# Optimization experiments

Measured on AMD Instinct MI355X. Metric: run time of the kernel, lower is better.

Reference implementation:

```python
import jax, jax.numpy as jnp
import numpy as np

TEMPERATURE = 0.1
NEG_FILL = -9e15


def setup_inputs() -> dict:
    key = jax.random.key(0)
    k1, k2, k3, k4 = jax.random.split(key, 4)
    N, D = 2048, 256
    loc1 = jax.random.normal(k1, (N, D), dtype=jnp.float32)
    loc2 = jax.random.normal(k3, (N, D), dtype=jnp.float32)
    # variances must be positive; sample in [0.5, 1.5)
    scale1 = jax.random.uniform(k2, (N, D), dtype=jnp.float32, minval=0.5, maxval=1.5)
    scale2 = jax.random.uniform(k4, (N, D), dtype=jnp.float32, minval=0.5, maxval=1.5)
    return {"loc1": loc1, "scale1": scale1, "loc2": loc2, "scale2": scale2}


def _kl_loss(loc1, scale1, loc2, scale2):
    N, D = loc1.shape
    mu = jnp.concatenate([loc1, loc2], axis=0)    # [2N, D]
    var = jnp.concatenate([scale1, scale2], axis=0)  # [2N, D] (treated as variance)
    inv_var = 1.0 / var
    s_logvar = jnp.sum(jnp.log(var), axis=-1)      # [2N]
    # kld[i,j] = 0.5 * sum_d( logvar_j - logvar_i - 1 + ((mu_i-mu_j)^2 + var_i)/var_j )
    # expand (mu_i-mu_j)^2 = mu_i^2 - 2 mu_i mu_j + mu_j^2 -> three GEMM/reduction terms
    a = (mu * mu + var) @ inv_var.T                # [2N,2N]: sum_d (mu_i^2+var_i)/var_j
    b = mu @ (mu * inv_var).T                      # [2N,2N]: sum_d mu_i mu_j / var_j
    c = jnp.sum(mu * mu * inv_var, axis=-1)        # [2N]:    sum_d mu_j^2 / var_j
    kld = 0.5 * (s_logvar[None, :] - s_logvar[:, None]
                 - jnp.float32(D) + a - 2.0 * b + c[None, :])
    M = 2 * N
    idx = jnp.arange(M)
    kld = kld.at[idx, idx].set(NEG_FILL)           # fill_diagonal_(-9e15)
    sim = kld / TEMPERATURE
    pos = sim[idx, (idx - N) % M]                  # eye rolled by N along dim 0
    loss = jax.nn.logsumexp(sim, axis=-1) - pos
    return jnp.mean(loss)


def reference(loc1, scale1, loc2, scale2):
    return _kl_loss(loc1, scale1, loc2, scale2)
```

## Files before the change

kernel.cpp:

```cpp
#include <hip/hip_runtime.h>
#include <hip/hip_bf16.h>
#include <math.h>

#define N_HALF 2048
#define M_TOT  4096
#define D_DIM  256
#define K2     512
#define NBLK   16
#define NKT    8
#define TILE_BYTES 32768

typedef __attribute__((ext_vector_type(8))) short bf16x8;
typedef __attribute__((ext_vector_type(4))) float f32x4;

static __device__ __forceinline__ unsigned short f2bf(float x) {
    union { __hip_bfloat16 h; unsigned short u; } cv;
    cv.h = __float2bfloat16(x);
    return cv.u;
}

static __device__ __forceinline__ void gll16(const void* g, void* l) {
    __builtin_amdgcn_global_load_lds(
        (const __attribute__((address_space(1))) unsigned int*)g,
        (__attribute__((address_space(3))) unsigned int*)l, 16, 0, 0);
}

#define FENCE asm volatile("" ::: "memory")
#define BAR() do { FENCE; __builtin_amdgcn_s_barrier(); FENCE; } while (0)
#define VM(n) asm volatile("s_waitcnt vmcnt(" #n ")" ::: "memory")

__global__ __launch_bounds__(256) void prep_kernel(
        const float* __restrict__ loc1, const float* __restrict__ scale1,
        const float* __restrict__ loc2, const float* __restrict__ scale2,
        unsigned short* __restrict__ Ab, unsigned short* __restrict__ Bb,
        float* __restrict__ slv, float* __restrict__ cvec,
        float* __restrict__ out) {
    const int t = threadIdx.x, w = t >> 6, lane = t & 63;
    if (blockIdx.x == 0 && t == 0) out[0] = 0.0f;
    const int i = blockIdx.x * 4 + w;
    const float* mup  = (i < N_HALF) ? loc1 + (size_t)i * D_DIM   : loc2 + (size_t)(i - N_HALF) * D_DIM;
    const float* vap  = (i < N_HALF) ? scale1 + (size_t)i * D_DIM : scale2 + (size_t)(i - N_HALF) * D_DIM;
    const float4 mu = *(const float4*)(mup + lane * 4);
    const float4 va = *(const float4*)(vap + lane * 4);
    const float4 iv = {1.0f / va.x, 1.0f / va.y, 1.0f / va.z, 1.0f / va.w};

    float lacc = __logf(va.x * va.y * va.z * va.w);
    float cacc = mu.x * mu.x * iv.x + mu.y * mu.y * iv.y
               + mu.z * mu.z * iv.z + mu.w * mu.w * iv.w;
    #pragma unroll
    for (int off = 1; off < 64; off <<= 1) {
        lacc += __shfl_xor(lacc, off, 64);
        cacc += __shfl_xor(cacc, off, 64);
    }
    if (lane == 0) { slv[i] = lacc; cvec[i] = cacc; }

    const int by = i >> 8, r = i & 255;
    const int rsw = (r >> 1) & 3;
    char* const abase = (char*)Ab + (size_t)by * (NKT * TILE_BYTES) + r * 64;
    char* const bbase = (char*)Bb + (size_t)by * (NKT * TILE_BYTES) + r * 64;
    #define ST4(base, k, v0, v1, v2, v3)                                             \
        {   const int kk = (k);                                                      \
            const int kt = kk >> 6, ks = (kk >> 5) & 1;                              \
            const int sl = ((kk >> 3) & 3) ^ rsw, hf = (kk >> 2) & 1;                \
            ushort4 pk = {f2bf(v0), f2bf(v1), f2bf(v2), f2bf(v3)};                   \
            *(ushort4*)((base) + (size_t)kt * TILE_BYTES + ks * 16384                \
                        + sl * 16 + hf * 8) = pk; }
    ST4(abase, lane * 4,          mu.x * mu.x + va.x, mu.y * mu.y + va.y,
                                  mu.z * mu.z + va.z, mu.w * mu.w + va.w)
    ST4(abase, 256 + lane * 4,    -2.0f * mu.x, -2.0f * mu.y, -2.0f * mu.z, -2.0f * mu.w)
    ST4(bbase, lane * 4,          iv.x, iv.y, iv.z, iv.w)
    ST4(bbase, 256 + lane * 4,    mu.x * iv.x, mu.y * iv.y, mu.z * iv.z, mu.w * iv.w)
    #undef ST4
}

__global__ __launch_bounds__(512, 2) void gemm_lse_kernel(
        const unsigned short* __restrict__ Ab, const unsigned short* __restrict__ Bb,
        const float* __restrict__ slv, const float* __restrict__ cvec,
        float* __restrict__ pm, float* __restrict__ ps,
        float* __restrict__ pos) {
    extern __shared__ __align__(16) char smem[];
    const int t = threadIdx.x;
    const int lane = t & 63, wid = t >> 6;
    const int bx = blockIdx.x, by = blockIdx.y;
    const int wrow = wid >> 2, wcol = wid & 3;
    const int fr = lane & 15, g = lane >> 4;
    const int t16 = t * 16;

    int a_off[8][2], b_off[4][2];
    #pragma unroll
    for (int fm = 0; fm < 8; ++fm) {
        const int row = wrow * 128 + fm * 16 + fr;
        #pragma unroll
        for (int ks = 0; ks < 2; ++ks)
            a_off[fm][ks] = ks * 16384 + row * 64 + ((g ^ ((row >> 1) & 3)) << 4);
    }
    #pragma unroll
    for (int fn = 0; fn < 4; ++fn) {
        const int row = wcol * 64 + fn * 16 + fr;
        #pragma unroll
        for (int ks = 0; ks < 2; ++ks)
            b_off[fn][ks] = 32768 + ks * 16384 + row * 64 + ((g ^ ((row >> 1) & 3)) << 4);
    }

    f32x4 acc[8][4];
    #pragma unroll
    for (int i = 0; i < 8; ++i)
        #pragma unroll
        for (int j = 0; j < 4; ++j) acc[i][j] = (f32x4){0.f, 0.f, 0.f, 0.f};

    const char* gA = (const char*)Ab + (size_t)by * (NKT * TILE_BYTES);
    const char* gB = (const char*)Bb + (size_t)bx * (NKT * TILE_BYTES);

    #define S2(kt, ks, isB)                                                          \
        {   const char* _s = ((isB) ? gB : gA) + (size_t)(kt) * TILE_BYTES           \
                             + (ks) * 16384;                                         \
            char* _d = smem + ((kt) & 1) * 65536 + ((isB) ? 32768 : 0)               \
                       + (ks) * 16384;                                               \
            gll16(_s + t16, _d + t16);                                               \
            gll16(_s + 8192 + t16, _d + 8192 + t16); }

    S2(0, 0, 0) S2(0, 0, 1) S2(0, 1, 0) S2(0, 1, 1) S2(1, 0, 0) S2(1, 0, 1)
    VM(8);
    BAR();

    bf16x8 bfr[4], af[8];
    for (int kt = 0; kt < NKT; ++kt) {
        const char* bufc = smem + (kt & 1) * 65536;

        #define MFMA16(FMH)                                                          \
            __builtin_amdgcn_s_setprio(1);                                           \
            _Pragma("unroll")                                                        \
            for (int q = 0; q < 4; ++q) {                                            \
                acc[(FMH)*4+q][0] = __builtin_amdgcn_mfma_f32_16x16x32_bf16(af[(FMH)*4+q], bfr[0], acc[(FMH)*4+q][0], 0, 0, 0); \
                acc[(FMH)*4+q][1] = __builtin_amdgcn_mfma_f32_16x16x32_bf16(af[(FMH)*4+q], bfr[1], acc[(FMH)*4+q][1], 0, 0, 0); \
                acc[(FMH)*4+q][2] = __builtin_amdgcn_mfma_f32_16x16x32_bf16(af[(FMH)*4+q], bfr[2], acc[(FMH)*4+q][2], 0, 0, 0); \
                acc[(FMH)*4+q][3] = __builtin_amdgcn_mfma_f32_16x16x32_bf16(af[(FMH)*4+q], bfr[3], acc[(FMH)*4+q][3], 0, 0, 0); \
            }                                                                        \
            __builtin_amdgcn_s_setprio(0);

        if (kt + 1 < NKT) S2(kt + 1, 1, 0)
        #pragma unroll
        for (int q = 0; q < 4; ++q) bfr[q]    = *(const bf16x8*)(bufc + b_off[q][0]);
        #pragma unroll
        for (int q = 0; q < 8; ++q) af[q]     = *(const bf16x8*)(bufc + a_off[q][0]);
        if (kt + 1 < NKT) S2(kt + 1, 1, 1)
        MFMA16(0)
        MFMA16(1)
        if (kt + 1 < NKT) { VM(8); } else { VM(0); }
        BAR();

        if (kt + 2 < NKT) S2(kt + 2, 0, 0)
        #pragma unroll
        for (int q = 0; q < 4; ++q) bfr[q]    = *(const bf16x8*)(bufc + b_off[q][1]);
        #pragma unroll
        for (int q = 0; q < 8; ++q) af[q]     = *(const bf16x8*)(bufc + a_off[q][1]);
        if (kt + 2 < NKT) S2(kt + 2, 0, 1)
        MFMA16(0)
        MFMA16(1)
        if (kt + 2 < NKT)      { VM(8); }
        else if (kt + 1 < NKT) { VM(4); }
        BAR();
        #undef MFMA16
    }
    #undef S2

    float colv[4]; int gcol[4];
    #pragma unroll
    for (int fn = 0; fn < 4; ++fn) {
        const int c = bx * 256 + wcol * 64 + fn * 16 + fr;
        gcol[fn] = c;
        colv[fn] = 5.0f * (slv[c] + cvec[c]) - 1280.0f;
    }
    float* redm = (float*)smem;
    float* reds = (float*)(smem + 4096);

    #pragma unroll
    for (int fm = 0; fm < 8; ++fm) {
        #pragma unroll
        for (int q = 0; q < 4; ++q) {
            const int rloc = wrow * 128 + fm * 16 + g * 4 + q;
            const int grow = by * 256 + rloc;
            const int jpart = grow ^ N_HALF;
            float v[4];
            #pragma unroll
            for (int fn = 0; fn < 4; ++fn) {
                const float x = 5.0f * acc[fm][fn][q] + colv[fn];
                if (gcol[fn] == jpart) pos[grow] = x;
                v[fn] = (grow == gcol[fn]) ? -3.0e38f : x;
            }
            float m = fmaxf(fmaxf(v[0], v[1]), fmaxf(v[2], v[3]));
            #pragma unroll
            for (int off = 1; off < 16; off <<= 1) m = fmaxf(m, __shfl_xor(m, off, 64));
            float s = __expf(v[0] - m) + __expf(v[1] - m) + __expf(v[2] - m) + __expf(v[3] - m);
            #pragma unroll
            for (int off = 1; off < 16; off <<= 1) s += __shfl_xor(s, off, 64);
            if (fr == 0) { redm[rloc * 4 + wcol] = m; reds[rloc * 4 + wcol] = s; }
        }
    }
    __syncthreads();
    if (t < 256) {
        float m = redm[t * 4], s = reds[t * 4];
        #pragma unroll
        for (int k = 1; k < 4; ++k) {
            const float mk = redm[t * 4 + k], sk = reds[t * 4 + k];
            const float nm = fmaxf(m, mk);
            s = s * __expf(m - nm) + sk * __expf(mk - nm);
            m = nm;
        }
        pm[(size_t)(by * 256 + t) * NBLK + bx] = m;
        ps[(size_t)(by * 256 + t) * NBLK + bx] = s;
    }
}

__global__ __launch_bounds__(256) void finalize_kernel(
        const float* __restrict__ pm, const float* __restrict__ ps,
        const float* __restrict__ pos, float* __restrict__ out) {
    __shared__ float sm[256];
    const int t = threadIdx.x;
    const int i = blockIdx.x * 256 + t;
    float mk[NBLK];
    float m = -3.0e38f;
    #pragma unroll
    for (int k = 0; k < NBLK; ++k) {
        mk[k] = pm[(size_t)i * NBLK + k];
        m = fmaxf(m, mk[k]);
    }
    float s = 0.0f;
    #pragma unroll
    for (int k = 0; k < NBLK; ++k)
        s += ps[(size_t)i * NBLK + k] * __expf(mk[k] - m);
    sm[t] = m + logf(s) - pos[i];
    __syncthreads();
    for (int off = 128; off > 0; off >>= 1) {
        if (t < off) sm[t] += sm[t + off];
        __syncthreads();
    }
    if (t == 0) atomicAdd(out, sm[0] * (1.0f / (float)M_TOT));
}

extern "C" void kernel_launch(void* const* d_in, const int* in_sizes, int n_in,
                              void* d_out, int out_size, void* d_ws, size_t ws_size,
                              hipStream_t stream) {
    const float* loc1   = (const float*)d_in[0];
    const float* scale1 = (const float*)d_in[1];
    const float* loc2   = (const float*)d_in[2];
    const float* scale2 = (const float*)d_in[3];
    float* out = (float*)d_out;

    char* ws = (char*)d_ws;
    unsigned short* Ab = (unsigned short*)ws;
    unsigned short* Bb = (unsigned short*)(ws + (size_t)4 * 1024 * 1024);
    float* slv  = (float*)(ws + (size_t)8 * 1024 * 1024);
    float* cvec = slv + M_TOT;
    float* pm   = cvec + M_TOT;
    float* ps   = pm + (size_t)M_TOT * NBLK;
    float* pos  = ps + (size_t)M_TOT * NBLK;

    hipLaunchKernelGGL(prep_kernel, dim3(M_TOT / 4), dim3(256), 0, stream,
                       loc1, scale1, loc2, scale2, Ab, Bb, slv, cvec, out);
    hipLaunchKernelGGL(gemm_lse_kernel, dim3(NBLK, NBLK), dim3(512), 131072, stream,
                       Ab, Bb, slv, cvec, pm, ps, pos);
    hipLaunchKernelGGL(finalize_kernel, dim3(NBLK), dim3(256), 0, stream,
                       pm, ps, pos, out);
}
```

Baseline: 42.30 us.

## Halve GEMM row tile, use 3-stage K pipeline and swizzled block order

The GEMM block tile changes from 256x256 to 128x256 with a K step of 32, doubling the grid to 512 blocks. Loads now go through a triple-buffered LDS ring of 24KB stages, and launch bounds rise to 4 blocks per CU. The prep kernel's packed bf16 layout is rewritten to match, and blocks are remapped so neighbouring blocks share B column tiles. The aim is to fill the 256 CUs better and hide load latency, at the cost of lower per-block reuse and more barriers per unit of work.

```diff
diff --git a/kernel.cpp b/kernel.cpp
--- a/kernel.cpp
+++ b/kernel.cpp
@@ -7,8 +7,11 @@
 #define D_DIM  256
 #define K2     512
 #define NBLK   16
-#define NKT    8
-#define TILE_BYTES 32768
+#define NKT    16
+#define A_TB   8192
+#define B_TB   16384
+#define BUF_B  24576
+#define NROWB  32
 
 typedef __attribute__((ext_vector_type(8))) short bf16x8;
 typedef __attribute__((ext_vector_type(4))) float f32x4;
@@ -54,26 +57,24 @@
     }
     if (lane == 0) { slv[i] = lacc; cvec[i] = cacc; }
 
-    const int by = i >> 8, r = i & 255;
-    const int rsw = (r >> 1) & 3;
-    char* const abase = (char*)Ab + (size_t)by * (NKT * TILE_BYTES) + r * 64;
-    char* const bbase = (char*)Bb + (size_t)by * (NKT * TILE_BYTES) + r * 64;
-    #define ST4(base, k, v0, v1, v2, v3)                                             \
+    const int rsw = (i >> 1) & 3;
+    char* const abase = (char*)Ab + (size_t)(i >> 7) * (NKT * A_TB) + (i & 127) * 64;
+    char* const bbase = (char*)Bb + (size_t)(i >> 8) * (NKT * B_TB) + (i & 255) * 64;
+    #define ST4(base, TB, k, v0, v1, v2, v3)                                         \
         {   const int kk = (k);                                                      \
-            const int kt = kk >> 6, ks = (kk >> 5) & 1;                              \
+            const int kt = kk >> 5;                                                  \
             const int sl = ((kk >> 3) & 3) ^ rsw, hf = (kk >> 2) & 1;                \
             ushort4 pk = {f2bf(v0), f2bf(v1), f2bf(v2), f2bf(v3)};                   \
-            *(ushort4*)((base) + (size_t)kt * TILE_BYTES + ks * 16384                \
-                        + sl * 16 + hf * 8) = pk; }
-    ST4(abase, lane * 4,          mu.x * mu.x + va.x, mu.y * mu.y + va.y,
-                                  mu.z * mu.z + va.z, mu.w * mu.w + va.w)
-    ST4(abase, 256 + lane * 4,    -2.0f * mu.x, -2.0f * mu.y, -2.0f * mu.z, -2.0f * mu.w)
-    ST4(bbase, lane * 4,          iv.x, iv.y, iv.z, iv.w)
-    ST4(bbase, 256 + lane * 4,    mu.x * iv.x, mu.y * iv.y, mu.z * iv.z, mu.w * iv.w)
+            *(ushort4*)((base) + (size_t)kt * (TB) + sl * 16 + hf * 8) = pk; }
+    ST4(abase, A_TB, lane * 4,       mu.x * mu.x + va.x, mu.y * mu.y + va.y,
+                                     mu.z * mu.z + va.z, mu.w * mu.w + va.w)
+    ST4(abase, A_TB, 256 + lane * 4, -2.0f * mu.x, -2.0f * mu.y, -2.0f * mu.z, -2.0f * mu.w)
+    ST4(bbase, B_TB, lane * 4,       iv.x, iv.y, iv.z, iv.w)
+    ST4(bbase, B_TB, 256 + lane * 4, mu.x * iv.x, mu.y * iv.y, mu.z * iv.z, mu.w * iv.w)
     #undef ST4
 }
 
-__global__ __launch_bounds__(512, 2) void gemm_lse_kernel(
+__global__ __launch_bounds__(512, 4) void gemm_lse_kernel(
         const unsigned short* __restrict__ Ab, const unsigned short* __restrict__ Bb,
         const float* __restrict__ slv, const float* __restrict__ cvec,
         float* __restrict__ pm, float* __restrict__ ps,
@@ -81,88 +82,72 @@
     extern __shared__ __align__(16) char smem[];
     const int t = threadIdx.x;
     const int lane = t & 63, wid = t >> 6;
-    const int bx = blockIdx.x, by = blockIdx.y;
+    const int bid = blockIdx.x;
+    const int swz = ((bid & 7) << 6) | (bid >> 3);
+    const int bx = swz >> 5, by2 = swz & 31;
     const int wrow = wid >> 2, wcol = wid & 3;
     const int fr = lane & 15, g = lane >> 4;
     const int t16 = t * 16;
 
-    int a_off[8][2], b_off[4][2];
-    #pragma unroll
-    for (int fm = 0; fm < 8; ++fm) {
-        const int row = wrow * 128 + fm * 16 + fr;
-        #pragma unroll
-        for (int ks = 0; ks < 2; ++ks)
-            a_off[fm][ks] = ks * 16384 + row * 64 + ((g ^ ((row >> 1) & 3)) << 4);
+    int a_off[4], b_off[4];
+    #pragma unroll
+    for (int fm = 0; fm < 4; ++fm) {
+        const int row = wrow * 64 + fm * 16 + fr;
+        a_off[fm] = row * 64 + ((g ^ ((row >> 1) & 3)) << 4);
     }
     #pragma unroll
     for (int fn = 0; fn < 4; ++fn) {
         const int row = wcol * 64 + fn * 16 + fr;
-        #pragma unroll
-        for (int ks = 0; ks < 2; ++ks)
-            b_off[fn][ks] = 32768 + ks * 16384 + row * 64 + ((g ^ ((row >> 1) & 3)) << 4);
-    }
-
-    f32x4 acc[8][4];
-    #pragma unroll
-    for (int i = 0; i < 8; ++i)
+        b_off[fn] = 8192 + row * 64 + ((g ^ ((row >> 1) & 3)) << 4);
+    }
+
+    f32x4 acc[4][4];
+    #pragma unroll
+    for (int i = 0; i < 4; ++i)
         #pragma unroll
         for (int j = 0; j < 4; ++j) acc[i][j] = (f32x4){0.f, 0.f, 0.f, 0.f};
 
-    const char* gA = (const char*)Ab + (size_t)by * (NKT * TILE_BYTES);
-    const char* gB = (const char*)Bb + (size_t)bx * (NKT * TILE_BYTES);
-
-    #define S2(kt, ks, isB)                                                          \
-        {   const char* _s = ((isB) ? gB : gA) + (size_t)(kt) * TILE_BYTES           \
-                             + (ks) * 16384;                                         \
-            char* _d = smem + ((kt) & 1) * 65536 + ((isB) ? 32768 : 0)               \
-                       + (ks) * 16384;                                               \
-            gll16(_s + t16, _d + t16);                                               \
-            gll16(_s + 8192 + t16, _d + 8192 + t16); }
-
-    S2(0, 0, 0) S2(0, 0, 1) S2(0, 1, 0) S2(0, 1, 1) S2(1, 0, 0) S2(1, 0, 1)
-    VM(8);
+    const char* gA = (const char*)Ab + (size_t)by2 * (NKT * A_TB);
+    const char* gB = (const char*)Bb + (size_t)bx * (NKT * B_TB);
+
+    #define STAGE(ktile, bidx)                                                       \
+        {   const char* _sA = gA + (size_t)(ktile) * A_TB;                           \
+            const char* _sB = gB + (size_t)(ktile) * B_TB;                           \
+            char* _d = smem + (bidx) * BUF_B;                                        \
+            gll16(_sA + t16,        _d + t16);                                       \
+            gll16(_sB + t16,        _d + 8192 + t16);                                \
+            gll16(_sB + 8192 + t16, _d + 16384 + t16); }
+
+    STAGE(0, 0)
+    STAGE(1, 1)
+    VM(3);
     BAR();
 
-    bf16x8 bfr[4], af[8];
+    int cur = 0;
+    bf16x8 bfr[4], af[4];
     for (int kt = 0; kt < NKT; ++kt) {
-        const char* bufc = smem + (kt & 1) * 65536;
-
-        #define MFMA16(FMH)                                                          \
-            __builtin_amdgcn_s_setprio(1);                                           \
-            _Pragma("unroll")                                                        \
-            for (int q = 0; q < 4; ++q) {                                            \
-                acc[(FMH)*4+q][0] = __builtin_amdgcn_mfma_f32_16x16x32_bf16(af[(FMH)*4+q], bfr[0], acc[(FMH)*4+q][0], 0, 0, 0); \
-                acc[(FMH)*4+q][1] = __builtin_amdgcn_mfma_f32_16x16x32_bf16(af[(FMH)*4+q], bfr[1], acc[(FMH)*4+q][1], 0, 0, 0); \
-                acc[(FMH)*4+q][2] = __builtin_amdgcn_mfma_f32_16x16x32_bf16(af[(FMH)*4+q], bfr[2], acc[(FMH)*4+q][2], 0, 0, 0); \
-                acc[(FMH)*4+q][3] = __builtin_amdgcn_mfma_f32_16x16x32_bf16(af[(FMH)*4+q], bfr[3], acc[(FMH)*4+q][3], 0, 0, 0); \
-            }                                                                        \
-            __builtin_amdgcn_s_setprio(0);
-
-        if (kt + 1 < NKT) S2(kt + 1, 1, 0)
-        #pragma unroll
-        for (int q = 0; q < 4; ++q) bfr[q]    = *(const bf16x8*)(bufc + b_off[q][0]);
-        #pragma unroll
-        for (int q = 0; q < 8; ++q) af[q]     = *(const bf16x8*)(bufc + a_off[q][0]);
-        if (kt + 1 < NKT) S2(kt + 1, 1, 1)
-        MFMA16(0)
-        MFMA16(1)
-        if (kt + 1 < NKT) { VM(8); } else { VM(0); }
+        const char* bufc = smem + cur * BUF_B;
+        int stg = cur + 2; if (stg >= 3) stg -= 3;
+        if (kt + 2 < NKT) STAGE(kt + 2, stg)
+        #pragma unroll
+        for (int q = 0; q < 4; ++q) bfr[q] = *(const bf16x8*)(bufc + b_off[q]);
+        #pragma unroll
+        for (int q = 0; q < 4; ++q) af[q]  = *(const bf16x8*)(bufc + a_off[q]);
+        __builtin_amdgcn_s_setprio(1);
+        #pragma unroll
+        for (int fm = 0; fm < 4; ++fm) {
+            acc[fm][0] = __builtin_amdgcn_mfma_f32_16x16x32_bf16(af[fm], bfr[0], acc[fm][0], 0, 0, 0);
+            acc[fm][1] = __builtin_amdgcn_mfma_f32_16x16x32_bf16(af[fm], bfr[1], acc[fm][1], 0, 0, 0);
+            acc[fm][2] = __builtin_amdgcn_mfma_f32_16x16x32_bf16(af[fm], bfr[2], acc[fm][2], 0, 0, 0);
+            acc[fm][3] = __builtin_amdgcn_mfma_f32_16x16x32_bf16(af[fm], bfr[3], acc[fm][3], 0, 0, 0);
+        }
+        __builtin_amdgcn_s_setprio(0);
+        if (kt + 2 < NKT)      { VM(3); }
+        else if (kt == NKT - 2) { VM(0); }
         BAR();
-
-        if (kt + 2 < NKT) S2(kt + 2, 0, 0)
-        #pragma unroll
-        for (int q = 0; q < 4; ++q) bfr[q]    = *(const bf16x8*)(bufc + b_off[q][1]);
-        #pragma unroll
-        for (int q = 0; q < 8; ++q) af[q]     = *(const bf16x8*)(bufc + a_off[q][1]);
-        if (kt + 2 < NKT) S2(kt + 2, 0, 1)
-        MFMA16(0)
-        MFMA16(1)
-        if (kt + 2 < NKT)      { VM(8); }
-        else if (kt + 1 < NKT) { VM(4); }
-        BAR();
-        #undef MFMA16
-    }
-    #undef S2
+        cur = (cur + 1 == 3) ? 0 : cur + 1;
+    }
+    #undef STAGE
 
     float colv[4]; int gcol[4];
     #pragma unroll
@@ -172,14 +157,14 @@
         colv[fn] = 5.0f * (slv[c] + cvec[c]) - 1280.0f;
     }
     float* redm = (float*)smem;
-    float* reds = (float*)(smem + 4096);
-
-    #pragma unroll
-    for (int fm = 0; fm < 8; ++fm) {
+    float* reds = (float*)(smem + 2048);
+
+    #pragma unroll
+    for (int fm = 0; fm < 4; ++fm) {
         #pragma unroll
         for (int q = 0; q < 4; ++q) {
-            const int rloc = wrow * 128 + fm * 16 + g * 4 + q;
-            const int grow = by * 256 + rloc;
+            const int rloc = wrow * 64 + fm * 16 + g * 4 + q;
+            const int grow = by2 * 128 + rloc;
             const int jpart = grow ^ N_HALF;
             float v[4];
             #pragma unroll
@@ -198,7 +183,7 @@
         }
     }
     __syncthreads();
-    if (t < 256) {
+    if (t < 128) {
         float m = redm[t * 4], s = reds[t * 4];
         #pragma unroll
         for (int k = 1; k < 4; ++k) {
@@ -207,8 +192,8 @@
             s = s * __expf(m - nm) + sk * __expf(mk - nm);
             m = nm;
         }
-        pm[(size_t)(by * 256 + t) * NBLK + bx] = m;
-        ps[(size_t)(by * 256 + t) * NBLK + bx] = s;
+        pm[(size_t)(by2 * 128 + t) * NBLK + bx] = m;
+        ps[(size_t)(by2 * 128 + t) * NBLK + bx] = s;
     }
 }
 
@@ -258,7 +243,7 @@
 
     hipLaunchKernelGGL(prep_kernel, dim3(M_TOT / 4), dim3(256), 0, stream,
                        loc1, scale1, loc2, scale2, Ab, Bb, slv, cvec, out);
-    hipLaunchKernelGGL(gemm_lse_kernel, dim3(NBLK, NBLK), dim3(512), 131072, stream,
+    hipLaunchKernelGGL(gemm_lse_kernel, dim3(NROWB * NBLK), dim3(512), 73728, stream,
                        Ab, Bb, slv, cvec, pm, ps, pos);
     hipLaunchKernelGGL(finalize_kernel, dim3(NBLK), dim3(256), 0, stream,
                        pm, ps, pos, out);
```

Measured after the change: 38.43 us. 1.1x faster.
